# Optimization experiments

Measured on AMD Instinct MI355X. Metric: run time of the kernel, lower is better.

## Reference

```python
import jax, jax.numpy as jnp
import numpy as np

EMB = 128      # config.emb_size
STEPS = 4      # config.mp_iterations
G = 64         # num_graphs
NPG = 1024     # nodes per graph (equal-size graphs, required by 'complete' branch)
NTOT = G * NPG
DEG = 8
E = NTOT * DEG


def _lrelu(x):
    return jax.nn.leaky_relu(x, 0.01)  # torch LeakyReLU default slope


def setup_inputs() -> dict:
    key = jax.random.key(0)
    ks = jax.random.split(key, 24)
    node_feats = jax.random.normal(ks[0], (NTOT, 5), jnp.float32)
    edge_attr = jax.random.normal(ks[1], (E, 4), jnp.float32)
    # edges constrained within each graph (block-diagonal), like Batch.from_data_list
    g = jnp.arange(E, dtype=jnp.int32) // (E // G)
    src = jax.random.randint(ks[2], (E,), 0, NPG, dtype=jnp.int32) + g * NPG
    dst = jax.random.randint(ks[3], (E,), 0, NPG, dtype=jnp.int32) + g * NPG
    edge_index = jnp.stack([src, dst])  # [2, E], row0 = source (j), row1 = target (i)
    batch_ind = jnp.arange(NTOT, dtype=jnp.int32) // NPG

    s = 0.05
    p = {}
    p["embed_W"] = jax.random.normal(ks[4], (5, EMB), jnp.float32) * s
    p["embed_b"] = jnp.zeros((EMB,), jnp.float32)
    p["mess_W"] = jax.random.normal(ks[5], (STEPS, EMB + 4, EMB), jnp.float32) * s
    p["mess_b"] = jnp.zeros((STEPS, EMB), jnp.float32)
    p["agg_W"] = jax.random.normal(ks[6], (STEPS, 3 * EMB, EMB), jnp.float32) * s
    p["agg_b"] = jnp.zeros((STEPS, EMB), jnp.float32)
    p["gate_W"] = jax.random.normal(ks[7], (STEPS, EMB, 1), jnp.float32) * s
    p["gate_b"] = jnp.zeros((STEPS, 1), jnp.float32)
    p["feat_W"] = jax.random.normal(ks[8], (STEPS, EMB, EMB), jnp.float32) * s
    p["feat_b"] = jnp.zeros((STEPS, EMB), jnp.float32)
    p["tr_W"] = jax.random.normal(ks[9], (STEPS, 2 * EMB, EMB), jnp.float32) * s
    p["tr_b"] = jnp.zeros((STEPS, EMB), jnp.float32)
    p["node_W"] = jax.random.normal(ks[10], (EMB, 5), jnp.float32) * s
    p["node_b"] = jnp.zeros((5,), jnp.float32)
    p["act_W"] = jax.random.normal(ks[11], (EMB, 5), jnp.float32) * s
    p["act_b"] = jnp.zeros((5,), jnp.float32)
    p["val_W"] = jax.random.normal(ks[12], (EMB, 1), jnp.float32) * s
    p["val_b"] = jnp.zeros((1,), jnp.float32)
    return dict(node_feats=node_feats, edge_attr=edge_attr, edge_index=edge_index,
                batch_ind=batch_ind, **p)


def reference(node_feats, edge_attr, edge_index, batch_ind,
              embed_W, embed_b, mess_W, mess_b, agg_W, agg_b,
              gate_W, gate_b, feat_W, feat_b, tr_W, tr_b,
              node_W, node_b, act_W, act_b, val_W, val_b):
    src, dst = edge_index[0], edge_index[1]
    # embed_node
    x = _lrelu(node_feats @ embed_W + embed_b)          # [N, EMB]
    xg = jnp.zeros((G, EMB), x.dtype)                   # x_global init

    for i in range(STEPS):
        # --- GraphNet: message (gather -> Linear+LeakyReLU) ---
        m = _lrelu(jnp.concatenate([x[src], edge_attr], axis=1) @ mess_W[i] + mess_b[i])  # [E, EMB]
        # scatter-max aggregation to target nodes; empty segments -> 0 (PyG behavior)
        agg = jax.ops.segment_max(m, dst, num_segments=NTOT)
        agg = jnp.where(jnp.isfinite(agg), agg, 0.0)
        # --- update: Linear+LeakyReLU + residual ---
        xgb = xg[batch_ind]                              # broadcast global per node
        x = _lrelu(jnp.concatenate([x, xgb, agg], axis=1) @ agg_W[i] + agg_b[i]) + x

        # --- GlobalNode: GlobalAttention pooling ---
        gate = (x @ gate_W[i] + gate_b[i])[:, 0]         # [N]
        gmax = jax.ops.segment_max(gate, batch_ind, num_segments=G)
        e = jnp.exp(gate - gmax[batch_ind])
        denom = jax.ops.segment_sum(e, batch_ind, num_segments=G)
        w = e / denom[batch_ind]                         # per-graph softmax weights
        feat = _lrelu(x @ feat_W[i] + feat_b[i])         # [N, EMB]
        xg_new = jax.ops.segment_sum(w[:, None] * feat, batch_ind, num_segments=G)
        xg = _lrelu(jnp.concatenate([xg_new, xg], axis=1) @ tr_W[i] + tr_b[i]) + xg

    # heads ('complete' branch)
    value = xg @ val_W + val_b                           # [G, 1]
    a_probs = jax.nn.softmax(xg @ act_W + act_b, axis=1) # [G, 5]
    node_act = (x @ node_W + node_b).reshape(G, NPG, 5)
    node_sm = jax.nn.softmax(node_act, axis=1)           # softmax over nodes per graph
    return a_probs, node_sm, value
```

## Files before the change

kernel.cpp:

```cpp
#include <hip/hip_runtime.h>
#include <hip/hip_bf16.h>

#define NTOT  65536
#define NE    524288
#define NG    64
#define NPG   1024
#define EMB   128
#define STEPS 4

typedef unsigned short u16;
typedef unsigned int   u32;
typedef __attribute__((ext_vector_type(8))) short          s16x8;
typedef __attribute__((ext_vector_type(8))) unsigned short us16x8;
typedef __attribute__((ext_vector_type(4))) float          f32x4;

__device__ __forceinline__ float lrelu(float v){ return v > 0.f ? v : 0.01f*v; }
__device__ __forceinline__ u16 f2bf(float f){
    u32 u = __float_as_uint(f);
    u32 r = (u + 0x7FFFu + ((u>>16)&1u)) >> 16;
    return (u16)r;
}
__device__ __forceinline__ float bf2f(u16 u){ return __uint_as_float(((u32)u)<<16); }
__device__ __forceinline__ void store_out(u32* out, int j, float v){
    u32 b = (u32)f2bf(v);
    out[j] = (b << 16) | b;
}

__global__ __launch_bounds__(256) void k_count(const int* __restrict__ dstv,
                                               u32* __restrict__ cnt){
    int e = blockIdx.x*256 + threadIdx.x;
    atomicAdd(&cnt[dstv[e]], 1u);
}

__global__ __launch_bounds__(1024) void k_scan(const u32* __restrict__ cnt,
                                               u32* __restrict__ off,
                                               u32* __restrict__ cursor){
    __shared__ u32 part[1024];
    int t = threadIdx.x;
    u32 s = 0;
    for (int i=0;i<64;i++) s += cnt[t*64+i];
    part[t] = s; __syncthreads();
    for (int d=1; d<1024; d<<=1){
        u32 v = (t>=d) ? part[t-d] : 0u;
        __syncthreads();
        part[t] += v;
        __syncthreads();
    }
    u32 base = (t==0) ? 0u : part[t-1];
    for (int i=0;i<64;i++){
        off[t*64+i] = base; cursor[t*64+i] = base;
        base += cnt[t*64+i];
    }
    if (t==1023) off[65536] = base;
}

__global__ __launch_bounds__(256) void k_scatter(const int* __restrict__ dstv,
                                                 u32* __restrict__ cursor,
                                                 u32* __restrict__ perm){
    int e = blockIdx.x*256 + threadIdx.x;
    u32 pos = atomicAdd(&cursor[dstv[e]], 1u);
    perm[pos] = e;
}

__global__ __launch_bounds__(256) void k_cvtw(const float* __restrict__ mW,
                        const float* __restrict__ aW, const float* __restrict__ fW,
                        u16* __restrict__ xwT, u16* __restrict__ waT,
                        u16* __restrict__ fwT){
    int idx = blockIdx.x*256 + threadIdx.x;
    int step = idx >> 16;
    int r = idx & 65535;
    if (r < 16384){
        int c = r>>7, k = r&127;
        xwT[step*16384 + r] = f2bf(mW[(size_t)step*132*EMB + (size_t)k*EMB + c]);
    } else if (r < 49152){
        int j = r-16384; int c = j>>8, k = j&255;
        int k2 = (k<128) ? k : (k+128);
        waT[step*32768 + j] = f2bf(aW[(size_t)step*384*EMB + (size_t)k2*EMB + c]);
    } else {
        int j = r-49152; int c = j>>7, k = j&127;
        fwT[step*16384 + j] = f2bf(fW[(size_t)step*EMB*EMB + (size_t)k*EMB + c]);
    }
}

__global__ __launch_bounds__(256) void k_embed(const float* __restrict__ nf,
                        const float* __restrict__ W,
                        const float* __restrict__ b, float* __restrict__ x,
                        u16* __restrict__ xb) {
    int idx = blockIdx.x*256 + threadIdx.x;
    int n = idx >> 7, c = idx & 127;
    const float* f = nf + n*5;
    float acc = b[c];
    #pragma unroll
    for (int k=0;k<5;k++) acc += f[k]*W[k*EMB+c];
    float v = lrelu(acc);
    x[idx] = v;
    xb[idx] = f2bf(v);
}

__global__ __launch_bounds__(256) void k_xwm(const u16* __restrict__ xb,
                        const u16* __restrict__ WT, const float* __restrict__ b,
                        u16* __restrict__ xwo) {
    int t = threadIdx.x, wv = t>>6, lane = t&63;
    int n0 = blockIdx.x*64;
    int row16 = lane&15, kg = lane>>4;
    f32x4 acc[8];
    #pragma unroll
    for (int ct=0;ct<8;ct++){
        float bc = b[ct*16+row16];
        acc[ct] = (f32x4){bc,bc,bc,bc};
    }
    for (int kt=0; kt<4; ++kt){
        s16x8 af = *(const s16x8*)(xb + (size_t)(n0+wv*16+row16)*EMB + kt*32 + kg*8);
        #pragma unroll
        for (int ct=0;ct<8;ct++){
            s16x8 bf = *(const s16x8*)(WT + (size_t)(ct*16+row16)*128 + kt*32 + kg*8);
            acc[ct] = __builtin_amdgcn_mfma_f32_16x16x32_bf16(af, bf, acc[ct], 0,0,0);
        }
    }
    #pragma unroll
    for (int ct=0;ct<8;ct++)
        #pragma unroll
        for (int reg=0;reg<4;reg++){
            int n = n0 + wv*16 + kg*4 + reg;
            xwo[(size_t)n*EMB + ct*16 + row16] = f2bf(acc[ct][reg]);
        }
}

__global__ __launch_bounds__(256) void k_msgmax2(const u16* __restrict__ xwb,
                          const float* __restrict__ ea,
                          const int* __restrict__ srcv,
                          const u32* __restrict__ off, const u32* __restrict__ perm,
                          const float* __restrict__ Wea,
                          u16* __restrict__ aggb) {
    int t = threadIdx.x;
    int le = t>>4, c = (t&15)*8;
    int n = blockIdx.x*16 + le;
    float we[4][8];
    #pragma unroll
    for (int r=0;r<4;r++)
        #pragma unroll
        for (int q=0;q<8;q++) we[r][q] = Wea[r*EMB + c + q];
    u32 j0 = off[n], j1 = off[n+1];
    float racc[8];
    #pragma unroll
    for (int q=0;q<8;q++) racc[q] = -INFINITY;
    for (u32 j=j0; j<j1; ++j){
        u32 e = perm[j];
        int s = srcv[e];
        const float4 ev = *(const float4*)(ea + (size_t)e*4);
        us16x8 xv = *(const us16x8*)(xwb + (size_t)s*EMB + c);
        #pragma unroll
        for (int q=0;q<8;q++){
            float m = bf2f(xv[q])
                    + ev.x*we[0][q] + ev.y*we[1][q] + ev.z*we[2][q] + ev.w*we[3][q];
            racc[q] = fmaxf(racc[q], lrelu(m));
        }
    }
    u16* o = aggb + (size_t)n*EMB + c;
    #pragma unroll
    for (int q=0;q<8;q++) o[q] = f2bf((racc[q] == -INFINITY) ? 0.f : racc[q]);
}

__global__ __launch_bounds__(256) void k_gemm1(float* __restrict__ x,
                        u16* __restrict__ xb,
                        const u16* __restrict__ aggb, const u16* __restrict__ WT,
                        const float* __restrict__ b, const float* __restrict__ xgw,
                        const float* __restrict__ gw, const float* __restrict__ gb,
                        float* __restrict__ w, float* __restrict__ denomp) {
    __shared__ float gred[16];
    int t = threadIdx.x, wv = t>>6, lane = t&63;
    int n0 = blockIdx.x*64, g = n0>>10;
    int row16 = lane&15, kg = lane>>4;
    f32x4 acc[8];
    #pragma unroll
    for (int ct=0;ct<8;ct++){
        int cc = ct*16+row16;
        float bc = b[cc] + xgw[g*EMB + cc];
        acc[ct] = (f32x4){bc,bc,bc,bc};
    }
    for (int kt=0; kt<8; ++kt){
        const u16* ap = (kt<4)
            ? xb   + (size_t)(n0+wv*16+row16)*EMB + kt*32 + kg*8
            : aggb + (size_t)(n0+wv*16+row16)*EMB + (kt-4)*32 + kg*8;
        s16x8 af = *(const s16x8*)ap;
        #pragma unroll
        for (int ct=0;ct<8;ct++){
            s16x8 bf = *(const s16x8*)(WT + (size_t)(ct*16+row16)*256 + kt*32 + kg*8);
            acc[ct] = __builtin_amdgcn_mfma_f32_16x16x32_bf16(af, bf, acc[ct], 0,0,0);
        }
    }
    float gpart[4] = {0.f,0.f,0.f,0.f};
    #pragma unroll
    for (int ct=0;ct<8;ct++){
        int cc = ct*16 + row16;
        float gwc = gw[cc];
        #pragma unroll
        for (int reg=0;reg<4;reg++){
            int n = n0 + wv*16 + kg*4 + reg;
            float v = lrelu(acc[ct][reg]) + x[(size_t)n*EMB + cc];
            x[(size_t)n*EMB + cc] = v;
            xb[(size_t)n*EMB + cc] = f2bf(v);
            gpart[reg] += v*gwc;
        }
    }
    #pragma unroll
    for (int o=1;o<16;o<<=1)
        #pragma unroll
        for (int reg=0;reg<4;reg++) gpart[reg] += __shfl_xor(gpart[reg], o);
    if (row16 == 0){
        float es = 0.f;
        #pragma unroll
        for (int reg=0;reg<4;reg++){
            float e = expf(gpart[reg] + gb[0]);
            w[n0 + wv*16 + kg*4 + reg] = e;
            es += e;
        }
        gred[wv*4 + kg] = es;
    }
    __syncthreads();
    if (t==0){
        float s = 0.f;
        #pragma unroll
        for (int i=0;i<16;i++) s += gred[i];
        denomp[blockIdx.x] = s;
    }
}

__global__ __launch_bounds__(256) void k_fx(const u16* __restrict__ xb,
                        const float* __restrict__ w,
                        const u16* __restrict__ fWT, const float* __restrict__ fb,
                        float* __restrict__ xgnp,
                        const u16* __restrict__ xWT, const float* __restrict__ mb,
                        u16* __restrict__ xwo) {
    __shared__ float red[4][128];
    int t = threadIdx.x, wv = t>>6, lane = t&63;
    int n0 = blockIdx.x*64;
    int row16 = lane&15, kg = lane>>4;
    bool doxw = (xWT != nullptr);
    f32x4 accf[8], accx[8];
    #pragma unroll
    for (int ct=0;ct<8;ct++){
        int cc = ct*16+row16;
        float fc = fb[cc];
        accf[ct] = (f32x4){fc,fc,fc,fc};
        float mc = doxw ? mb[cc] : 0.f;
        accx[ct] = (f32x4){mc,mc,mc,mc};
    }
    for (int kt=0; kt<4; ++kt){
        s16x8 af = *(const s16x8*)(xb + (size_t)(n0+wv*16+row16)*EMB + kt*32 + kg*8);
        #pragma unroll
        for (int ct=0;ct<8;ct++){
            s16x8 bff = *(const s16x8*)(fWT + (size_t)(ct*16+row16)*128 + kt*32 + kg*8);
            accf[ct] = __builtin_amdgcn_mfma_f32_16x16x32_bf16(af, bff, accf[ct], 0,0,0);
        }
        if (doxw){
            #pragma unroll
            for (int ct=0;ct<8;ct++){
                s16x8 bfx = *(const s16x8*)(xWT + (size_t)(ct*16+row16)*128 + kt*32 + kg*8);
                accx[ct] = __builtin_amdgcn_mfma_f32_16x16x32_bf16(af, bfx, accx[ct], 0,0,0);
            }
        }
    }
    float e[4];
    #pragma unroll
    for (int reg=0;reg<4;reg++) e[reg] = w[n0 + wv*16 + kg*4 + reg];
    #pragma unroll
    for (int ct=0;ct<8;ct++){
        float p = 0.f;
        #pragma unroll
        for (int reg=0;reg<4;reg++){
            p += e[reg]*lrelu(accf[ct][reg]);
            if (doxw){
                int n = n0 + wv*16 + kg*4 + reg;
                xwo[(size_t)n*EMB + ct*16 + row16] = f2bf(accx[ct][reg]);
            }
        }
        p += __shfl_xor(p, 16);
        p += __shfl_xor(p, 32);
        if (kg == 0) red[wv][ct*16 + row16] = p;
    }
    __syncthreads();
    if (t < 128){
        float s = red[0][t]+red[1][t]+red[2][t]+red[3][t];
        xgnp[(size_t)blockIdx.x*128 + t] = s;
    }
}

__global__ __launch_bounds__(128) void k_tr(float* __restrict__ xg,
                     const float* __restrict__ xgnp, const float* __restrict__ denomp,
                     const float* __restrict__ W, const float* __restrict__ b,
                     const float* __restrict__ W2next, float* __restrict__ xgw) {
    __shared__ float in[256];
    __shared__ float xgs[128];
    int g = blockIdx.x, t = threadIdx.x;
    float s = 0.f, d = 0.f;
    for (int j=0;j<16;j++){
        s += xgnp[(size_t)(g*16+j)*128 + t];
        d += denomp[g*16+j];
    }
    in[t]     = s/d;
    in[128+t] = xg[g*EMB + t];
    __syncthreads();
    float acc = b[t];
    for (int k=0;k<256;k++) acc += in[k]*W[(size_t)k*EMB + t];
    float xgnew = lrelu(acc) + in[128+t];
    xg[g*EMB+t] = xgnew;
    xgs[t] = xgnew;
    __syncthreads();
    if (W2next){
        float a2 = 0.f;
        for (int k=0;k<EMB;k++) a2 += xgs[k]*W2next[(size_t)k*EMB + t];
        xgw[g*EMB + t] = a2;
    }
}

__global__ __launch_bounds__(64) void k_ghead(const float* __restrict__ xg,
                        const float* __restrict__ actW, const float* __restrict__ actb,
                        const float* __restrict__ valW, const float* __restrict__ valb,
                        u32* __restrict__ out) {
    int g = blockIdx.x, l = threadIdx.x;
    float xa = xg[g*EMB + l], xb = xg[g*EMB + 64 + l];
    float acc[6];
    #pragma unroll
    for (int o=0;o<5;o++) acc[o] = xa*actW[l*5+o] + xb*actW[(l+64)*5+o];
    acc[5] = xa*valW[l] + xb*valW[64+l];
    #pragma unroll
    for (int o=0;o<6;o++){
        float sv = acc[o];
        #pragma unroll
        for (int d=1;d<64;d<<=1) sv += __shfl_xor(sv, d);
        acc[o] = sv;
    }
    if (l==0){
        float lg[5], m = -1e30f;
        #pragma unroll
        for (int o=0;o<5;o++){ lg[o]=acc[o]+actb[o]; m = fmaxf(m, lg[o]); }
        float ssum=0.f;
        #pragma unroll
        for (int o=0;o<5;o++){ lg[o]=expf(lg[o]-m); ssum+=lg[o]; }
        float inv = 1.f/ssum;
        #pragma unroll
        for (int o=0;o<5;o++) store_out(out, g*5+o, lg[o]*inv);
        store_out(out, 328000 + g, acc[5] + valb[0]);
    }
}

__global__ __launch_bounds__(256) void k_nlog(const float* __restrict__ x,
                       const float* __restrict__ W,
                       const float* __restrict__ b, float* __restrict__ nl) {
    int n = blockIdx.x*256 + threadIdx.x;
    const float4* xr = (const float4*)(x + (size_t)n*EMB);
    float acc[5] = {b[0],b[1],b[2],b[3],b[4]};
    for (int k=0;k<32;k++){
        float4 v4 = xr[k];
        #pragma unroll
        for (int jj=0;jj<4;jj++){
            float v = (&v4.x)[jj];
            int k4 = k*4+jj;
            #pragma unroll
            for (int o=0;o<5;o++) acc[o] += v*W[k4*5+o];
        }
    }
    #pragma unroll
    for (int o=0;o<5;o++) nl[(size_t)n*5+o] = acc[o];
}

__global__ __launch_bounds__(256) void k_nodesm(const float* __restrict__ nl,
                         u32* __restrict__ out) {
    __shared__ float red[5][4];
    int g = blockIdx.x, t = threadIdx.x;
    float v[4][5];
    #pragma unroll
    for (int it=0; it<4; ++it){
        int n = g*NPG + it*256 + t;
        #pragma unroll
        for (int o=0;o<5;o++) v[it][o] = nl[(size_t)n*5+o];
    }
    float m[5];
    #pragma unroll
    for (int o=0;o<5;o++){
        float mm = fmaxf(fmaxf(v[0][o],v[1][o]),fmaxf(v[2][o],v[3][o]));
        #pragma unroll
        for (int d=1;d<64;d<<=1) mm = fmaxf(mm, __shfl_xor(mm,d));
        if ((t&63)==0) red[o][t>>6] = mm;
    }
    __syncthreads();
    #pragma unroll
    for (int o=0;o<5;o++)
        m[o] = fmaxf(fmaxf(red[o][0],red[o][1]),fmaxf(red[o][2],red[o][3]));
    __syncthreads();
    #pragma unroll
    for (int o=0;o<5;o++){
        float ss = 0.f;
        #pragma unroll
        for (int it=0;it<4;it++){ v[it][o] = expf(v[it][o]-m[o]); ss += v[it][o]; }
        #pragma unroll
        for (int d=1;d<64;d<<=1) ss += __shfl_xor(ss,d);
        if ((t&63)==0) red[o][t>>6] = ss;
    }
    __syncthreads();
    float s[5];
    #pragma unroll
    for (int o=0;o<5;o++)
        s[o] = 1.f/(red[o][0]+red[o][1]+red[o][2]+red[o][3]);
    #pragma unroll
    for (int it=0;it<4;it++){
        int n = g*NPG + it*256 + t;
        #pragma unroll
        for (int o=0;o<5;o++)
            store_out(out, 320 + n*5 + o, v[it][o]*s[o]);
    }
}

extern "C" void kernel_launch(void* const* d_in, const int* in_sizes, int n_in,
                              void* d_out, int out_size, void* d_ws, size_t ws_size,
                              hipStream_t stream) {
    const float* node_feats = (const float*)d_in[0];
    const float* edge_attr  = (const float*)d_in[1];
    const int*   edge_index = (const int*)d_in[2];
    const float* embed_W = (const float*)d_in[4];
    const float* embed_b = (const float*)d_in[5];
    const float* mess_W  = (const float*)d_in[6];
    const float* mess_b  = (const float*)d_in[7];
    const float* agg_W   = (const float*)d_in[8];
    const float* agg_b   = (const float*)d_in[9];
    const float* gate_W  = (const float*)d_in[10];
    const float* gate_b  = (const float*)d_in[11];
    const float* feat_W  = (const float*)d_in[12];
    const float* feat_b  = (const float*)d_in[13];
    const float* tr_W    = (const float*)d_in[14];
    const float* tr_b    = (const float*)d_in[15];
    const float* node_W  = (const float*)d_in[16];
    const float* node_b  = (const float*)d_in[17];
    const float* act_W   = (const float*)d_in[18];
    const float* act_b   = (const float*)d_in[19];
    const float* val_W   = (const float*)d_in[20];
    const float* val_b   = (const float*)d_in[21];

    char* ws = (char*)d_ws;
    float* x      = (float*)(ws);
    u16*   aggb   = (u16*)(ws + 33554432);
    float* nl     = (float*)(ws + 33554432);
    u16*   xb     = (u16*)(ws + 50331648);
    u32* cnt      = (u32*)(ws + 67108864);
    u32* off      = (u32*)(ws + 67108864 + 1048576);
    u32* cursor   = (u32*)(ws + 67108864 + 2097152);
    u32* perm     = (u32*)(ws + 67108864 + 3145728);
    float* xgw    = (float*)(ws + 73400320);
    float* denomp = (float*)(ws + 73400320 + 32768);
    float* w      = (float*)(ws + 73400320 + 65536);
    float* xgnp   = (float*)(ws + 73400320 + 327680);
    u16*   xwb    = (u16*)(ws + 75497472);
    u16*   xwT    = (u16*)(ws + 92274688);
    u16*   waT    = (u16*)(ws + 92274688 + 131072);
    u16*   fwT    = (u16*)(ws + 92274688 + 393216);
    u32* out = (u32*)d_out;
    float* xg     = (float*)((char*)d_out + 4096);

    const int* srcv = edge_index;
    const int* dstv = edge_index + NE;

    hipMemsetAsync(cnt, 0, NTOT*sizeof(u32), stream);
    k_count  <<<NE/256, 256, 0, stream>>>(dstv, cnt);
    k_scan   <<<1, 1024, 0, stream>>>(cnt, off, cursor);
    k_scatter<<<NE/256, 256, 0, stream>>>(dstv, cursor, perm);

    hipMemsetAsync(xg, 0, NG*EMB*sizeof(float), stream);
    hipMemsetAsync(xgw, 0, NG*EMB*sizeof(float), stream);
    k_cvtw<<<1024, 256, 0, stream>>>(mess_W, agg_W, feat_W, xwT, waT, fwT);
    k_embed<<<NTOT*EMB/256, 256, 0, stream>>>(node_feats, embed_W, embed_b, x, xb);
    k_xwm<<<NTOT/64, 256, 0, stream>>>(xb, xwT, mess_b, xwb);

    for (int i=0;i<STEPS;i++){
        bool last = (i+1 >= STEPS);
        k_msgmax2<<<NTOT/16, 256, 0, stream>>>(xwb, edge_attr, srcv, off, perm,
            mess_W + (size_t)i*132*EMB + (size_t)128*EMB, aggb);
        k_gemm1<<<NTOT/64, 256, 0, stream>>>(x, xb, aggb, waT + (size_t)i*32768,
            agg_b + i*EMB, xgw, gate_W + i*EMB, gate_b + i, w, denomp);
        k_fx<<<NTOT/64, 256, 0, stream>>>(xb, w, fwT + (size_t)i*16384,
            feat_b + i*EMB, xgnp,
            last ? nullptr : (xwT + (size_t)(i+1)*16384),
            last ? nullptr : (mess_b + (i+1)*EMB), xwb);
        k_tr<<<NG, 128, 0, stream>>>(xg, xgnp, denomp,
            tr_W + (size_t)i*256*EMB, tr_b + i*EMB,
            last ? nullptr : (agg_W + (size_t)(i+1)*384*EMB + (size_t)128*EMB), xgw);
    }

    k_ghead<<<NG, 64, 0, stream>>>(xg, act_W, act_b, val_W, val_b, out);
    k_nlog<<<NTOT/256, 256, 0, stream>>>(x, node_W, node_b, nl);
    k_nodesm<<<NG, 256, 0, stream>>>(nl, out);
}
```

Before: 763.7 us.

## Swizzle block-to-graph mapping across XCDs and unroll edge gather by two

Remaps block indices in the node kernels so that every block of a given graph lands on the same XCD (block index mod 8). Each graph's node rows, and the source rows that message passing gathers, then stay in one XCD's L2. The per-block partial sums in k_tr are re-indexed to match the new layout. The edge max-aggregation loop is also unrolled by two so that two independent gathers are in flight at once. The cost is slightly more complex indexing, and the code now assumes the 8-XCD layout and these fixed sizes.

```diff
diff --git a/kernel.cpp b/kernel.cpp
--- a/kernel.cpp
+++ b/kernel.cpp
@@ -97,11 +97,18 @@
     xb[idx] = f2bf(v);
 }
 
+__device__ __forceinline__ int swz_n0_1024(int p){
+    int xcd = p & 7, j = p >> 3;
+    int gi = j >> 4, wi = j & 15;
+    int g = gi*8 + xcd;
+    return (g*16 + wi)*64;
+}
+
 __global__ __launch_bounds__(256) void k_xwm(const u16* __restrict__ xb,
                         const u16* __restrict__ WT, const float* __restrict__ b,
                         u16* __restrict__ xwo) {
     int t = threadIdx.x, wv = t>>6, lane = t&63;
-    int n0 = blockIdx.x*64;
+    int n0 = swz_n0_1024(blockIdx.x);
     int row16 = lane&15, kg = lane>>4;
     f32x4 acc[8];
     #pragma unroll
@@ -132,9 +139,13 @@
                           const u32* __restrict__ off, const u32* __restrict__ perm,
                           const float* __restrict__ Wea,
                           u16* __restrict__ aggb) {
+    int p = blockIdx.x;
+    int xcd = p & 7, j = p >> 3;
+    int gi = j >> 6, wi = j & 63;
+    int g = gi*8 + xcd;
     int t = threadIdx.x;
     int le = t>>4, c = (t&15)*8;
-    int n = blockIdx.x*16 + le;
+    int n = (g*64 + wi)*16 + le;
     float we[4][8];
     #pragma unroll
     for (int r=0;r<4;r++)
@@ -144,16 +155,33 @@
     float racc[8];
     #pragma unroll
     for (int q=0;q<8;q++) racc[q] = -INFINITY;
-    for (u32 j=j0; j<j1; ++j){
-        u32 e = perm[j];
-        int s = srcv[e];
-        const float4 ev = *(const float4*)(ea + (size_t)e*4);
-        us16x8 xv = *(const us16x8*)(xwb + (size_t)s*EMB + c);
+    u32 jj = j0;
+    for (; jj+2 <= j1; jj += 2){
+        u32 e0 = perm[jj], e1 = perm[jj+1];
+        int s0 = srcv[e0], s1 = srcv[e1];
+        const float4 ev0 = *(const float4*)(ea + (size_t)e0*4);
+        const float4 ev1 = *(const float4*)(ea + (size_t)e1*4);
+        us16x8 xv0 = *(const us16x8*)(xwb + (size_t)s0*EMB + c);
+        us16x8 xv1 = *(const us16x8*)(xwb + (size_t)s1*EMB + c);
         #pragma unroll
         for (int q=0;q<8;q++){
-            float m = bf2f(xv[q])
-                    + ev.x*we[0][q] + ev.y*we[1][q] + ev.z*we[2][q] + ev.w*we[3][q];
-            racc[q] = fmaxf(racc[q], lrelu(m));
+            float m0 = bf2f(xv0[q])
+                     + ev0.x*we[0][q] + ev0.y*we[1][q] + ev0.z*we[2][q] + ev0.w*we[3][q];
+            float m1 = bf2f(xv1[q])
+                     + ev1.x*we[0][q] + ev1.y*we[1][q] + ev1.z*we[2][q] + ev1.w*we[3][q];
+            racc[q] = fmaxf(racc[q], fmaxf(lrelu(m0), lrelu(m1)));
+        }
+    }
+    if (jj < j1){
+        u32 e0 = perm[jj];
+        int s0 = srcv[e0];
+        const float4 ev0 = *(const float4*)(ea + (size_t)e0*4);
+        us16x8 xv0 = *(const us16x8*)(xwb + (size_t)s0*EMB + c);
+        #pragma unroll
+        for (int q=0;q<8;q++){
+            float m0 = bf2f(xv0[q])
+                     + ev0.x*we[0][q] + ev0.y*we[1][q] + ev0.z*we[2][q] + ev0.w*we[3][q];
+            racc[q] = fmaxf(racc[q], lrelu(m0));
         }
     }
     u16* o = aggb + (size_t)n*EMB + c;
@@ -169,7 +197,8 @@
                         float* __restrict__ w, float* __restrict__ denomp) {
     __shared__ float gred[16];
     int t = threadIdx.x, wv = t>>6, lane = t&63;
-    int n0 = blockIdx.x*64, g = n0>>10;
+    int n0 = swz_n0_1024(blockIdx.x);
+    int g = n0>>10;
     int row16 = lane&15, kg = lane>>4;
     f32x4 acc[8];
     #pragma unroll
@@ -234,7 +263,7 @@
                         u16* __restrict__ xwo) {
     __shared__ float red[4][128];
     int t = threadIdx.x, wv = t>>6, lane = t&63;
-    int n0 = blockIdx.x*64;
+    int n0 = swz_n0_1024(blockIdx.x);
     int row16 = lane&15, kg = lane>>4;
     bool doxw = (xWT != nullptr);
     f32x4 accf[8], accx[8];
@@ -294,9 +323,10 @@
     __shared__ float xgs[128];
     int g = blockIdx.x, t = threadIdx.x;
     float s = 0.f, d = 0.f;
-    for (int j=0;j<16;j++){
-        s += xgnp[(size_t)(g*16+j)*128 + t];
-        d += denomp[g*16+j];
+    for (int wi=0; wi<16; wi++){
+        int p = (g&7) + 8*((g>>3)*16 + wi);
+        s += xgnp[(size_t)p*128 + t];
+        d += denomp[p];
     }
     in[t]     = s/d;
     in[128+t] = xg[g*EMB + t];
```

New measurement: 743.3 us. 1.03x faster.
